# Optimization experiments

Hardware: AMD Instinct MI355X
Metric: run time of the kernel (lower is better)

## Reference

```python
import jax, jax.numpy as jnp
import numpy as np

N = 20000      # nodes
E = 256000     # edges
H = 8          # heads
DIN = 256      # in_dim_struct / in_dim_semantic
DH = 32        # num_hidden per head (H*DH == DIN for GT residual)
PRED = 32      # pred_dim (relation embedding dim)
REL = 16       # rel_num
NEG = 0.2      # negative_slope for GAT attention
ALPHA = 0.5    # args.fusion
NUM_LAYERS = 2


def seg_softmax(e, seg, n):
    # softmax over edges grouped by destination node; e: [E, ...], seg: [E]
    m = jax.ops.segment_max(e, seg, num_segments=n)
    ex = jnp.exp(e - m[seg])
    s = jax.ops.segment_sum(ex, seg, num_segments=n)
    return ex / (s[seg] + 1e-9)


def setup_inputs() -> dict:
    key = jax.random.key(0)
    ks = jax.random.split(key, 24)
    f32 = jnp.float32
    def rn(k, shape, scale=0.05):
        return jax.random.normal(k, shape, dtype=f32) * scale
    return {
        "feats_struct": jax.random.normal(ks[0], (N, DIN), f32),
        "feats_semantic": jax.random.normal(ks[1], (N, DIN), f32),
        "centrality": jax.random.uniform(ks[2], (N,), f32),
        # fused per-head scoring MLP (heads[0] small Sequentials batched over H)
        "Ws1": rn(ks[3], (H, DIN, DIN // 2)),
        "bs1": jnp.zeros((H, DIN // 2), f32),
        "Ws2": rn(ks[4], (H, DIN // 2)),
        "bs2": jnp.zeros((H,), f32),
        "rel_emb": rn(ks[5], (REL, PRED), 1.0),
        # SALayer params (2 layers, per-head scalar channels)
        "sa_w": rn(ks[6], (NUM_LAYERS, H), 1.0),
        "sa_al": rn(ks[7], (NUM_LAYERS, H), 1.0),
        "sa_ar": rn(ks[8], (NUM_LAYERS, H), 1.0),
        "sa_We": rn(ks[9], (NUM_LAYERS, PRED, H)),
        # GTLayer params
        "Wq": rn(ks[10], (DIN, H * DH)),
        "bq": jnp.zeros((H * DH,), f32),
        "Wk": rn(ks[11], (DIN, H * DH)),
        "bk": jnp.zeros((H * DH,), f32),
        "Wv": rn(ks[12], (DIN, H * DH)),
        "bv": jnp.zeros((H * DH,), f32),
        "We_gt": rn(ks[13], (PRED, H * DH)),
        "bn_gamma": jnp.ones((H * DH,), f32),
        "bn_beta": jnp.zeros((H * DH,), f32),
        "Wout": rn(ks[14], (H * DH, 1)),
        "bout": jnp.zeros((1,), f32),
        # centrality scale params
        "gamma": jnp.ones((1, H), f32),
        "beta": jnp.zeros((1, H), f32),
        "edge_types": jax.random.randint(ks[15], (E,), 0, REL),
        "edge_src": jax.random.randint(ks[16], (E,), 0, N),
        "edge_dst": jax.random.randint(ks[17], (E,), 0, N),
    }


def _forward(feats_struct, feats_semantic, centrality, Ws1, bs1, Ws2, bs2,
             rel_emb, sa_w, sa_al, sa_ar, sa_We, Wq, bq, Wk, bk, Wv, bv,
             We_gt, bn_gamma, bn_beta, Wout, bout, gamma, beta,
             edge_types, edge_src, edge_dst):
    n = feats_struct.shape[0]
    edge_feats = rel_emb[edge_types]                                   # [E, PRED]

    # ---- structural channel: fused per-head scoring MLPs ----
    h1 = jax.nn.relu(jnp.einsum('nd,hdk->nhk', feats_struct, Ws1) + bs1)  # [N,H,DIN/2]
    h = jnp.einsum('nhk,hk->nh', h1, Ws2) + bs2                           # [N,H]

    # ---- SALayer stack (GAT-style, per-head scalar features) ----
    for l in range(NUM_LAYERS):
        z = h * sa_w[l]                                                 # [N,H]
        e = jax.nn.leaky_relu(z[edge_src] * sa_al[l] + z[edge_dst] * sa_ar[l]
                              + edge_feats @ sa_We[l], NEG)             # [E,H]
        attn = seg_softmax(e, edge_dst, n)                              # [E,H]
        out = jax.ops.segment_sum(attn * z[edge_src], edge_dst, num_segments=n)
        h = jax.nn.elu(out + z)                                         # residual + activation
        if l != NUM_LAYERS - 1:
            h = jnp.mean(h, axis=-1, keepdims=True)
            h = jnp.tile(h, (1, H))
    logits_struct = h                                                   # [N,H]

    # ---- semantic channel: Graph Transformer layer (edge_mode='MUL') ----
    q = (feats_semantic @ Wq + bq).reshape(n, H, DH)
    k = (feats_semantic @ Wk + bk).reshape(n, H, DH)
    v = (feats_semantic @ Wv + bv).reshape(n, H, DH)
    ep = (edge_feats @ We_gt).reshape(-1, H, DH)                        # [E,H,DH]
    ke = k[edge_src] * ep                                               # MUL edge gating
    score = jnp.sum(q[edge_dst] * ke, axis=-1) / jnp.sqrt(jnp.float32(DH))  # [E,H]
    attn = seg_softmax(score, edge_dst, n)                              # [E,H]
    agg = jax.ops.segment_sum(attn[..., None] * v[edge_src], edge_dst,
                              num_segments=n).reshape(n, H * DH)
    agg = agg + feats_semantic                                          # residual (H*DH == DIN)
    mu = jnp.mean(agg, axis=0)
    var = jnp.var(agg, axis=0)
    agg = (agg - mu) / jnp.sqrt(var + 1e-5) * bn_gamma + bn_beta        # batch norm
    h_sem = jax.nn.relu(agg)
    logits_semantic = h_sem @ Wout + bout                               # [N,1]

    # ---- fusion + centrality gamma/beta scaling ----
    logits = ALPHA * logits_struct + (1.0 - ALPHA) * logits_semantic    # [N,H]
    scaled = (centrality[:, None] * gamma + beta) * logits              # [N,H]
    return jax.nn.leaky_relu(jnp.mean(scaled, axis=-1, keepdims=True), 0.01)


def reference(feats_struct, feats_semantic, centrality, Ws1, bs1, Ws2, bs2,
              rel_emb, sa_w, sa_al, sa_ar, sa_We, Wq, bq, Wk, bk, Wv, bv,
              We_gt, bn_gamma, bn_beta, Wout, bout, gamma, beta,
              edge_types, edge_src, edge_dst):
    return _forward(feats_struct, feats_semantic, centrality, Ws1, bs1, Ws2, bs2,
                    rel_emb, sa_w, sa_al, sa_ar, sa_We, Wq, bq, Wk, bk, Wv, bv,
                    We_gt, bn_gamma, bn_beta, Wout, bout, gamma, beta,
                    edge_types, edge_src, edge_dst)
```

## Files before the change

### kernel.cpp

```cpp
#include <hip/hip_runtime.h>
#include <hip/hip_bf16.h>
#include <math.h>

#define N_NODES 20000
#define N_EDGES 256000
#define LOG2E 1.4426950408889634f

typedef __attribute__((ext_vector_type(8))) __bf16 bf16x8;
typedef __attribute__((ext_vector_type(8))) unsigned short u16x8;
typedef __attribute__((ext_vector_type(4))) float f32x4;

static __device__ __forceinline__ unsigned short f2bf(float f) {
  unsigned u = __float_as_uint(f);
  unsigned r = (u + 0x7fffu + ((u >> 16) & 1u)) >> 16;
  return (unsigned short)r;
}
static __device__ __forceinline__ float b2f(unsigned short u) {
  return __uint_as_float((unsigned)u << 16);
}

__global__ __launch_bounds__(256) void k_setup(
    const float* __restrict__ rel_emb, const float* __restrict__ sa_We,
    const float* __restrict__ We_gt, const float* __restrict__ Xs,
    const float* __restrict__ Xm, const float* __restrict__ Ws1,
    const float* __restrict__ Wq, const float* __restrict__ Wk,
    const float* __restrict__ Wv, const int* __restrict__ e_dst,
    float* __restrict__ saTab, float* __restrict__ epTab,
    ushort* __restrict__ Xsb, ushort* __restrict__ Xmb,
    ushort* __restrict__ Ws1t, ushort* __restrict__ Wt,
    int* __restrict__ deg) {
  int b = blockIdx.x;
  int t = threadIdx.x;
  if (b == 0) {
    {
      int l = t >> 7, r = (t >> 3) & 15, h = t & 7;
      float acc = 0.f;
      for (int p = 0; p < 32; ++p)
        acc += rel_emb[r * 32 + p] * sa_We[l * 256 + p * 8 + h];
      saTab[t] = acc * LOG2E;
    }
    for (int r = 0; r < 16; ++r) {
      float acc = 0.f;
      for (int p = 0; p < 32; ++p)
        acc += rel_emb[r * 32 + p] * We_gt[p * 256 + t];
      epTab[r * 256 + t] = acc;
    }
  } else if (b < 5001) {
    size_t i = ((size_t)(b - 1) * 256 + t) * 4;
    float4 a = *(const float4*)(Xs + i);
    ushort4 ua = {f2bf(a.x), f2bf(a.y), f2bf(a.z), f2bf(a.w)};
    *(ushort4*)(Xsb + i) = ua;
    float4 c = *(const float4*)(Xm + i);
    ushort4 uc = {f2bf(c.x), f2bf(c.y), f2bf(c.z), f2bf(c.w)};
    *(ushort4*)(Xmb + i) = uc;
  } else if (b < 6025) {
    int lb = b - 5001;
    int h = lb >> 7, kcol = lb & 127;
    Ws1t[((size_t)h * 128 + kcol) * 256 + t] =
        f2bf(Ws1[((size_t)h * 256 + t) * 128 + kcol]);
  } else if (b < 6793) {
    int lb = b - 6025;
    int m = lb >> 8, n = lb & 255;
    const float* W = (m == 0) ? Wq : (m == 1) ? Wk : Wv;
    Wt[((size_t)m * 256 + n) * 256 + t] = f2bf(W[(size_t)t * 256 + n]);
  } else {
    int e = (b - 6793) * 256 + t;
    if (e < N_EDGES) atomicAdd(&deg[e_dst[e]], 1);
  }
}

__global__ __launch_bounds__(1024) void k_scan(const int* __restrict__ deg,
                                               int* __restrict__ rowPtr,
                                               int* __restrict__ cursor) {
  const int CH = (N_NODES + 1023) / 1024;
  int t = threadIdx.x;
  int b0 = t * CH, b1 = min(b0 + CH, N_NODES);
  int s = 0;
  for (int i = b0; i < b1; ++i) s += deg[i];
  __shared__ int part[1024];
  part[t] = s;
  __syncthreads();
  for (int off = 1; off < 1024; off <<= 1) {
    int add = (t >= off) ? part[t - off] : 0;
    __syncthreads();
    part[t] += add;
    __syncthreads();
  }
  int run = (t == 0) ? 0 : part[t - 1];
  for (int i = b0; i < b1; ++i) {
    rowPtr[i] = run;
    cursor[i] = run;
    run += deg[i];
  }
  if (t == 0) rowPtr[N_NODES] = part[1023];
}

__global__ void k_fill(const int* __restrict__ e_dst, const int* __restrict__ e_src,
                       const int* __restrict__ e_type, int* __restrict__ cursor,
                       int2* __restrict__ csrPack) {
  int e = blockIdx.x * 256 + threadIdx.x;
  if (e >= N_EDGES) return;
  int d = e_dst[e];
  int pos = atomicAdd(&cursor[d], 1);
  csrPack[pos] = make_int2(e_src[e], e_type[e]);
}

__global__ __launch_bounds__(256) void k_gemm(
    const ushort* __restrict__ Xsb, const ushort* __restrict__ Xmb,
    const ushort* __restrict__ Ws1t, const ushort* __restrict__ Wqkvt,
    const float* __restrict__ bs1, const float* __restrict__ Ws2,
    const float* __restrict__ bs2, const float* __restrict__ bq,
    const float* __restrict__ bk, const float* __restrict__ bv,
    float* __restrict__ h0, float* __restrict__ q, ushort* __restrict__ kvB) {
  __shared__ ushort Ab[64][136];
  __shared__ ushort Bb[128][136];
  int tid = threadIdx.x;
  int y = blockIdx.y;
  bool isMlp = (y < 8);
  int m = 0, half = 0;
  const ushort* Bsrc;
  const ushort* Xb;
  if (isMlp) {
    Xb = Xsb;
    Bsrc = Ws1t + (size_t)y * 128 * 256;
  } else {
    m = (y - 8) >> 1;
    half = (y - 8) & 1;
    Xb = Xmb;
    Bsrc = Wqkvt + ((size_t)m * 256 + half * 128) * 256;
  }
  int base = blockIdx.x * 64;
  int wv = tid >> 6, lane = tid & 63;
  int l15 = lane & 15, lhi = lane >> 4;
  f32x4 acc[8];
  #pragma unroll
  for (int nt = 0; nt < 8; ++nt) acc[nt] = (f32x4){0.f, 0.f, 0.f, 0.f};

  for (int kc = 0; kc < 2; ++kc) {
    {
      int r = tid >> 2, c4 = (tid & 3) * 4;
      int gr = base + r;
      const ushort* src = Xb + (size_t)gr * 256 + kc * 128;
      #pragma unroll
      for (int s = 0; s < 4; ++s) {
        u16x8 val = {0, 0, 0, 0, 0, 0, 0, 0};
        if (gr < N_NODES) val = *(const u16x8*)(src + (c4 + s) * 8);
        *(u16x8*)&Ab[r][(c4 + s) * 8] = val;
      }
    }
    {
      int r = tid >> 1, cb = (tid & 1) * 8;
      const ushort* src = Bsrc + (size_t)r * 256 + kc * 128;
      #pragma unroll
      for (int s = 0; s < 8; ++s)
        *(u16x8*)&Bb[r][(cb + s) * 8] = *(const u16x8*)(src + (cb + s) * 8);
    }
    __syncthreads();
    #pragma unroll
    for (int kk = 0; kk < 4; ++kk) {
      bf16x8 a = *(const bf16x8*)&Ab[wv * 16 + l15][kk * 32 + lhi * 8];
      #pragma unroll
      for (int nt = 0; nt < 8; ++nt) {
        bf16x8 b = *(const bf16x8*)&Bb[nt * 16 + l15][kk * 32 + lhi * 8];
        acc[nt] = __builtin_amdgcn_mfma_f32_16x16x32_bf16(a, b, acc[nt], 0, 0, 0);
      }
    }
    __syncthreads();
  }

  if (isMlp) {
    float part[4] = {0.f, 0.f, 0.f, 0.f};
    #pragma unroll
    for (int nt = 0; nt < 8; ++nt) {
      int c = y * 128 + nt * 16 + l15;
      float b1 = bs1[c], w2 = Ws2[c];
      #pragma unroll
      for (int j = 0; j < 4; ++j)
        part[j] += fmaxf(acc[nt][j] + b1, 0.f) * w2;
    }
    #pragma unroll
    for (int j = 0; j < 4; ++j) {
      #pragma unroll
      for (int o = 1; o < 16; o <<= 1) part[j] += __shfl_xor(part[j], o);
    }
    if (l15 == 0) {
      float b2 = bs2[y];
      #pragma unroll
      for (int j = 0; j < 4; ++j) {
        int row = base + wv * 16 + lhi * 4 + j;
        if (row < N_NODES) h0[(size_t)row * 8 + y] = part[j] + b2;
      }
    }
  } else {
    const float* bias = (m == 0) ? bq : (m == 1) ? bk : bv;
    #pragma unroll
    for (int nt = 0; nt < 8; ++nt) {
      int c = half * 128 + nt * 16 + l15;
      float bc = bias[c];
      #pragma unroll
      for (int j = 0; j < 4; ++j) {
        int row = base + wv * 16 + lhi * 4 + j;
        if (row < N_NODES) {
          float val = acc[nt][j] + bc;
          if (m == 0) q[(size_t)row * 256 + c] = val;
          else if (m == 1) kvB[(size_t)row * 512 + c] = f2bf(val);
          else kvB[(size_t)row * 512 + 256 + c] = f2bf(val);
        }
      }
    }
  }
}


__global__ __launch_bounds__(256) void k_sa(const float* __restrict__ h_in,
                                            float* __restrict__ h_out,
                                            const int* __restrict__ rowPtr,
                                            const int2* __restrict__ csrPack,
                                            const float* __restrict__ sa_w,
                                            const float* __restrict__ sa_al,
                                            const float* __restrict__ sa_ar,
                                            const float* __restrict__ saTab, int layer) {
  int node = blockIdx.x * 4 + (threadIdx.x >> 6);
  int lane = threadIdx.x & 63;
  int h = lane & 7, eslot = lane >> 3;
  float wgt = sa_w[layer * 8 + h];
  float al2 = sa_al[layer * 8 + h] * LOG2E;
  float ar2 = sa_ar[layer * 8 + h] * LOG2E;
  const float* tab = saTab + layer * 128;
  float zd = h_in[(size_t)node * 8 + h] * wgt;
  int s0 = rowPtr[node], s1 = rowPtr[node + 1];
  float m = -1e30f, lsum = 0.f, acc = 0.f;
  for (int i = s0 + eslot; i < s1; i += 8) {
    int2 p = csrPack[i];
    float zs = h_in[(size_t)p.x * 8 + h] * wgt;
    float e = zs * al2 + zd * ar2 + tab[p.y * 8 + h];
    e = (e >= 0.f) ? e : 0.2f * e;
    float nm = fmaxf(m, e);
    float scl = exp2f(m - nm);
    float pw = exp2f(e - nm);
    acc = acc * scl + pw * zs;
    lsum = lsum * scl + pw;
    m = nm;
  }
  #pragma unroll
  for (int off = 8; off < 64; off <<= 1) {
    float om = __shfl_xor(m, off);
    float ol = __shfl_xor(lsum, off);
    float oa = __shfl_xor(acc, off);
    float nm = fmaxf(m, om);
    float sl = exp2f(m - nm);
    float so = exp2f(om - nm);
    acc = acc * sl + oa * so;
    lsum = lsum * sl + ol * so;
    m = nm;
  }
  float o = acc / (lsum + 1e-9f);
  float r = o + zd;
  r = (r > 0.f) ? r : expm1f(r);
  if (layer == 0) {
    r += __shfl_xor(r, 1);
    r += __shfl_xor(r, 2);
    r += __shfl_xor(r, 4);
    r *= 0.125f;
  }
  if (eslot == 0) h_out[(size_t)node * 8 + h] = r;
}


__global__ __launch_bounds__(256) void k_gt(const float* __restrict__ q,
                                            const ushort* __restrict__ kvB,
                                            const float* __restrict__ epTab,
                                            const float* __restrict__ feats_sem,
                                            const int* __restrict__ rowPtr,
                                            const int2* __restrict__ csrPack,
                                            ushort* __restrict__ agg) {
  int node = blockIdx.x * 4 + (threadIdx.x >> 6);
  int lane = threadIdx.x & 63;
  int c0 = lane * 4;
  const float SC2 = 0.17677669529663687f * LOG2E;
  float4 qv = *(const float4*)(q + (size_t)node * 256 + c0);
  qv.x *= SC2; qv.y *= SC2; qv.z *= SC2; qv.w *= SC2;
  float4 acc = {0.f, 0.f, 0.f, 0.f};
  float m = -1e30f, lsum = 0.f;
  int s0 = rowPtr[node], s1 = rowPtr[node + 1];
  int i = s0;
  for (; i + 1 < s1; i += 2) {
    int2 eA = csrPack[i], eB = csrPack[i + 1];
    const ushort* rA = kvB + (size_t)eA.x * 512 + c0;
    const ushort* rB = kvB + (size_t)eB.x * 512 + c0;
    ushort4 kA = *(const ushort4*)rA;
    ushort4 kB4 = *(const ushort4*)rB;
    float4 epA = *(const float4*)(epTab + eA.y * 256 + c0);
    float4 epB = *(const float4*)(epTab + eB.y * 256 + c0);
    ushort4 vA = *(const ushort4*)(rA + 256);
    ushort4 vB = *(const ushort4*)(rB + 256);
    float pA = qv.x * b2f(kA.x) * epA.x + qv.y * b2f(kA.y) * epA.y +
               qv.z * b2f(kA.z) * epA.z + qv.w * b2f(kA.w) * epA.w;
    float pB = qv.x * b2f(kB4.x) * epB.x + qv.y * b2f(kB4.y) * epB.y +
               qv.z * b2f(kB4.z) * epB.z + qv.w * b2f(kB4.w) * epB.w;
    pA += __shfl_xor(pA, 1); pB += __shfl_xor(pB, 1);
    pA += __shfl_xor(pA, 2); pB += __shfl_xor(pB, 2);
    pA += __shfl_xor(pA, 4); pB += __shfl_xor(pB, 4);
    float nm = fmaxf(m, fmaxf(pA, pB));
    float scl = exp2f(m - nm);
    float wA = exp2f(pA - nm);
    float wB = exp2f(pB - nm);
    acc.x = acc.x * scl + wA * b2f(vA.x) + wB * b2f(vB.x);
    acc.y = acc.y * scl + wA * b2f(vA.y) + wB * b2f(vB.y);
    acc.z = acc.z * scl + wA * b2f(vA.z) + wB * b2f(vB.z);
    acc.w = acc.w * scl + wA * b2f(vA.w) + wB * b2f(vB.w);
    lsum = lsum * scl + wA + wB;
    m = nm;
  }
  if (i < s1) {
    int2 eA = csrPack[i];
    const ushort* rA = kvB + (size_t)eA.x * 512 + c0;
    ushort4 kv = *(const ushort4*)rA;
    float4 ep = *(const float4*)(epTab + eA.y * 256 + c0);
    ushort4 vv = *(const ushort4*)(rA + 256);
    float part = qv.x * b2f(kv.x) * ep.x + qv.y * b2f(kv.y) * ep.y +
                 qv.z * b2f(kv.z) * ep.z + qv.w * b2f(kv.w) * ep.w;
    part += __shfl_xor(part, 1);
    part += __shfl_xor(part, 2);
    part += __shfl_xor(part, 4);
    float nm = fmaxf(m, part);
    float scl = exp2f(m - nm);
    float pw = exp2f(part - nm);
    acc.x = acc.x * scl + pw * b2f(vv.x);
    acc.y = acc.y * scl + pw * b2f(vv.y);
    acc.z = acc.z * scl + pw * b2f(vv.z);
    acc.w = acc.w * scl + pw * b2f(vv.w);
    lsum = lsum * scl + pw;
    m = nm;
  }
  float inv = 1.f / (lsum + 1e-9f);
  float4 fs = *(const float4*)(feats_sem + (size_t)node * 256 + c0);
  ushort4 r;
  r.x = f2bf(acc.x * inv + fs.x);
  r.y = f2bf(acc.y * inv + fs.y);
  r.z = f2bf(acc.z * inv + fs.z);
  r.w = f2bf(acc.w * inv + fs.w);
  *(ushort4*)(agg + (size_t)node * 256 + c0) = r;
}

__global__ void k_bnstats(const ushort* __restrict__ agg, double* __restrict__ colsum,
                          double* __restrict__ colssq) {
  int t = threadIdx.x;
  int r0 = blockIdx.x * 79;
  int r1 = min(r0 + 79, N_NODES);
  double s = 0.0, qq = 0.0;
  for (int r = r0; r < r1; ++r) {
    float x = b2f(agg[(size_t)r * 256 + t]);
    s += (double)x;
    qq += (double)x * (double)x;
  }
  atomicAdd(&colsum[t], s);
  atomicAdd(&colssq[t], qq);
}

__global__ void k_bnfinal(const double* __restrict__ colsum, const double* __restrict__ colssq,
                          float* __restrict__ muArr, float* __restrict__ invArr) {
  int t = threadIdx.x;
  double mu = colsum[t] / (double)N_NODES;
  double var = colssq[t] / (double)N_NODES - mu * mu;
  muArr[t] = (float)mu;
  invArr[t] = (float)(1.0 / sqrt(var + 1e-5));
}

__global__ __launch_bounds__(256) void k_final(const ushort* __restrict__ agg,
                                               const float* __restrict__ muArr,
                                               const float* __restrict__ invArr,
                                               const float* __restrict__ bn_gamma,
                                               const float* __restrict__ bn_beta,
                                               const float* __restrict__ Wout,
                                               const float* __restrict__ bout,
                                               const float* __restrict__ hB,
                                               const float* __restrict__ cent,
                                               const float* __restrict__ gamma,
                                               const float* __restrict__ beta,
                                               float* __restrict__ out) {
  int node = blockIdx.x * 4 + (threadIdx.x >> 6);
  int lane = threadIdx.x & 63;
  int c0 = lane * 4;
  ushort4 xa = *(const ushort4*)(agg + (size_t)node * 256 + c0);
  float4 mu = *(const float4*)(muArr + c0);
  float4 iv = *(const float4*)(invArr + c0);
  float4 g = *(const float4*)(bn_gamma + c0);
  float4 b = *(const float4*)(bn_beta + c0);
  float4 w = *(const float4*)(Wout + c0);
  float p = fmaxf((b2f(xa.x) - mu.x) * iv.x * g.x + b.x, 0.f) * w.x +
            fmaxf((b2f(xa.y) - mu.y) * iv.y * g.y + b.y, 0.f) * w.y +
            fmaxf((b2f(xa.z) - mu.z) * iv.z * g.z + b.z, 0.f) * w.z +
            fmaxf((b2f(xa.w) - mu.w) * iv.w * g.w + b.w, 0.f) * w.w;
  #pragma unroll
  for (int o = 1; o < 64; o <<= 1) p += __shfl_xor(p, o);
  float ls = p + bout[0];
  int h = lane & 7;
  float logit = 0.5f * hB[(size_t)node * 8 + h] + 0.5f * ls;
  float sc = (cent[node] * gamma[h] + beta[h]) * logit;
  sc += __shfl_xor(sc, 1);
  sc += __shfl_xor(sc, 2);
  sc += __shfl_xor(sc, 4);
  float mn = sc * 0.125f;
  mn = (mn >= 0.f) ? mn : 0.01f * mn;
  if (lane == 0) out[node] = mn;
}


extern "C" void kernel_launch(void* const* d_in, const int* in_sizes, int n_in,
                              void* d_out, int out_size, void* d_ws, size_t ws_size,
                              hipStream_t stream) {
  (void)in_sizes; (void)n_in; (void)out_size; (void)ws_size;
  const float* feats_struct = (const float*)d_in[0];
  const float* feats_sem    = (const float*)d_in[1];
  const float* cent         = (const float*)d_in[2];
  const float* Ws1          = (const float*)d_in[3];
  const float* bs1          = (const float*)d_in[4];
  const float* Ws2          = (const float*)d_in[5];
  const float* bs2          = (const float*)d_in[6];
  const float* rel_emb      = (const float*)d_in[7];
  const float* sa_w         = (const float*)d_in[8];
  const float* sa_al        = (const float*)d_in[9];
  const float* sa_ar        = (const float*)d_in[10];
  const float* sa_We        = (const float*)d_in[11];
  const float* Wq           = (const float*)d_in[12];
  const float* bq           = (const float*)d_in[13];
  const float* Wk           = (const float*)d_in[14];
  const float* bk           = (const float*)d_in[15];
  const float* Wv           = (const float*)d_in[16];
  const float* bv           = (const float*)d_in[17];
  const float* We_gt        = (const float*)d_in[18];
  const float* bn_gamma     = (const float*)d_in[19];
  const float* bn_beta      = (const float*)d_in[20];
  const float* Wout         = (const float*)d_in[21];
  const float* bout         = (const float*)d_in[22];
  const float* gamma        = (const float*)d_in[23];
  const float* beta         = (const float*)d_in[24];
  const int* e_type         = (const int*)d_in[25];
  const int* e_src          = (const int*)d_in[26];
  const int* e_dst          = (const int*)d_in[27];
  float* out = (float*)d_out;

  char* wsb = (char*)d_ws;
  size_t off = 0;
  auto alloc = [&](size_t bytes) -> char* {
    char* p = wsb + off;
    off = (off + bytes + 255) & ~(size_t)255;
    return p;
  };
  float* saTab   = (float*)alloc(2 * 16 * 8 * 4);
  float* epTab   = (float*)alloc(16 * 256 * 4);
  int* deg       = (int*)alloc((size_t)N_NODES * 4);
  int* rowPtr    = (int*)alloc((size_t)(N_NODES + 1) * 4);
  int* cursor    = (int*)alloc((size_t)N_NODES * 4);
  int2* csrPack  = (int2*)alloc((size_t)N_EDGES * 8);
  float* h0      = (float*)alloc((size_t)N_NODES * 8 * 4);
  float* hA      = (float*)alloc((size_t)N_NODES * 8 * 4);
  float* hB      = (float*)alloc((size_t)N_NODES * 8 * 4);
  float* qb      = (float*)alloc((size_t)N_NODES * 256 * 4);
  ushort* kvB    = (ushort*)alloc((size_t)N_NODES * 512 * 2);
  ushort* agg    = (ushort*)alloc((size_t)N_NODES * 256 * 2);
  double* colsum = (double*)alloc(256 * 8);
  double* colssq = (double*)alloc(256 * 8);
  float* muArr   = (float*)alloc(256 * 4);
  float* invArr  = (float*)alloc(256 * 4);
  ushort* Xsb    = (ushort*)alloc((size_t)N_NODES * 256 * 2);
  ushort* Xmb    = (ushort*)alloc((size_t)N_NODES * 256 * 2);
  ushort* Ws1t   = (ushort*)alloc((size_t)8 * 128 * 256 * 2);
  ushort* Wqkvt  = (ushort*)alloc((size_t)3 * 256 * 256 * 2);

  hipMemsetAsync(deg, 0, (size_t)N_NODES * 4, stream);
  hipMemsetAsync(colsum, 0, 256 * 8, stream);
  hipMemsetAsync(colssq, 0, 256 * 8, stream);

  k_setup<<<7793, 256, 0, stream>>>(rel_emb, sa_We, We_gt, feats_struct, feats_sem,
                                    Ws1, Wq, Wk, Wv, e_dst,
                                    saTab, epTab, Xsb, Xmb, Ws1t, Wqkvt, deg);
  k_scan<<<1, 1024, 0, stream>>>(deg, rowPtr, cursor);
  k_fill<<<(N_EDGES + 255) / 256, 256, 0, stream>>>(e_dst, e_src, e_type, cursor, csrPack);

  const int MT = (N_NODES + 63) / 64;
  dim3 gGemm(MT, 14);
  k_gemm<<<gGemm, 256, 0, stream>>>(Xsb, Xmb, Ws1t, Wqkvt, bs1, Ws2, bs2,
                                    bq, bk, bv, h0, qb, kvB);
  k_sa<<<(N_NODES + 3) / 4, 256, 0, stream>>>(h0, hA, rowPtr, csrPack,
                                              sa_w, sa_al, sa_ar, saTab, 0);
  k_sa<<<(N_NODES + 3) / 4, 256, 0, stream>>>(hA, hB, rowPtr, csrPack,
                                              sa_w, sa_al, sa_ar, saTab, 1);
  k_gt<<<N_NODES / 4, 256, 0, stream>>>(qb, kvB, epTab, feats_sem,
                                        rowPtr, csrPack, agg);
  k_bnstats<<<256, 256, 0, stream>>>(agg, colsum, colssq);
  k_bnfinal<<<1, 256, 0, stream>>>(colsum, colssq, muArr, invArr);
  k_final<<<N_NODES / 4, 256, 0, stream>>>(agg, muArr, invArr, bn_gamma, bn_beta,
                                           Wout, bout, hB, cent, gamma, beta, out);
}
```

Baseline: 367.1 us.

## Enlarge GEMM M-tile to 128 rows and swizzle LDS to avoid bank conflicts

The fused MLP/QKV GEMM kernel now processes 128 rows per block instead of 64, with each wave computing two 16-row MFMA tiles that share each B fragment, so B reuse doubles and weight tile reloads are halved. LDS padding is replaced by an XOR swizzle on the column index to cut bank conflicts while keeping a dense 128-wide layout. The cost is more accumulator registers per thread and half as many blocks in the grid, which lowers parallelism for a 20000-row problem.

```diff
diff --git a/kernel.cpp b/kernel.cpp
--- a/kernel.cpp
+++ b/kernel.cpp
@@ -112,8 +112,8 @@
     const float* __restrict__ bs2, const float* __restrict__ bq,
     const float* __restrict__ bk, const float* __restrict__ bv,
     float* __restrict__ h0, float* __restrict__ q, ushort* __restrict__ kvB) {
-  __shared__ ushort Ab[64][136];
-  __shared__ ushort Bb[128][136];
+  __shared__ ushort Ab[128][128];
+  __shared__ ushort Bb[128][128];
   int tid = threadIdx.x;
   int y = blockIdx.y;
   bool isMlp = (y < 8);
@@ -129,67 +129,78 @@
     Xb = Xmb;
     Bsrc = Wqkvt + ((size_t)m * 256 + half * 128) * 256;
   }
-  int base = blockIdx.x * 64;
+  int base = blockIdx.x * 128;
   int wv = tid >> 6, lane = tid & 63;
   int l15 = lane & 15, lhi = lane >> 4;
-  f32x4 acc[8];
+  int rs = tid >> 4;
+  int cs = (tid & 15) * 8;
+  f32x4 acc[2][8];
   #pragma unroll
-  for (int nt = 0; nt < 8; ++nt) acc[nt] = (f32x4){0.f, 0.f, 0.f, 0.f};
+  for (int mr = 0; mr < 2; ++mr)
+    #pragma unroll
+    for (int nt = 0; nt < 8; ++nt) acc[mr][nt] = (f32x4){0.f, 0.f, 0.f, 0.f};
 
   for (int kc = 0; kc < 2; ++kc) {
-    {
-      int r = tid >> 2, c4 = (tid & 3) * 4;
+    #pragma unroll
+    for (int s = 0; s < 8; ++s) {
+      int r = rs + s * 16;
+      int csw = cs ^ ((r & 7) << 3);
       int gr = base + r;
-      const ushort* src = Xb + (size_t)gr * 256 + kc * 128;
-      #pragma unroll
-      for (int s = 0; s < 4; ++s) {
-        u16x8 val = {0, 0, 0, 0, 0, 0, 0, 0};
-        if (gr < N_NODES) val = *(const u16x8*)(src + (c4 + s) * 8);
-        *(u16x8*)&Ab[r][(c4 + s) * 8] = val;
-      }
-    }
-    {
-      int r = tid >> 1, cb = (tid & 1) * 8;
-      const ushort* src = Bsrc + (size_t)r * 256 + kc * 128;
-      #pragma unroll
-      for (int s = 0; s < 8; ++s)
-        *(u16x8*)&Bb[r][(cb + s) * 8] = *(const u16x8*)(src + (cb + s) * 8);
+      u16x8 val = {0, 0, 0, 0, 0, 0, 0, 0};
+      if (gr < N_NODES) val = *(const u16x8*)(Xb + (size_t)gr * 256 + kc * 128 + cs);
+      *(u16x8*)&Ab[r][csw] = val;
+    }
+    #pragma unroll
+    for (int s = 0; s < 8; ++s) {
+      int r = rs + s * 16;
+      int csw = cs ^ ((r & 7) << 3);
+      *(u16x8*)&Bb[r][csw] = *(const u16x8*)(Bsrc + (size_t)r * 256 + kc * 128 + cs);
     }
     __syncthreads();
+    int swzA = (l15 & 7) << 3;
     #pragma unroll
     for (int kk = 0; kk < 4; ++kk) {
-      bf16x8 a = *(const bf16x8*)&Ab[wv * 16 + l15][kk * 32 + lhi * 8];
+      int col = (kk * 32 + lhi * 8);
+      bf16x8 a0 = *(const bf16x8*)&Ab[wv * 32 + l15][col ^ swzA];
+      bf16x8 a1 = *(const bf16x8*)&Ab[wv * 32 + 16 + l15][col ^ swzA];
       #pragma unroll
       for (int nt = 0; nt < 8; ++nt) {
-        bf16x8 b = *(const bf16x8*)&Bb[nt * 16 + l15][kk * 32 + lhi * 8];
-        acc[nt] = __builtin_amdgcn_mfma_f32_16x16x32_bf16(a, b, acc[nt], 0, 0, 0);
+        bf16x8 b = *(const bf16x8*)&Bb[nt * 16 + l15][col ^ swzA];
+        acc[0][nt] = __builtin_amdgcn_mfma_f32_16x16x32_bf16(a0, b, acc[0][nt], 0, 0, 0);
+        acc[1][nt] = __builtin_amdgcn_mfma_f32_16x16x32_bf16(a1, b, acc[1][nt], 0, 0, 0);
       }
     }
     __syncthreads();
   }
 
   if (isMlp) {
-    float part[4] = {0.f, 0.f, 0.f, 0.f};
+    float part[2][4] = {{0.f, 0.f, 0.f, 0.f}, {0.f, 0.f, 0.f, 0.f}};
     #pragma unroll
     for (int nt = 0; nt < 8; ++nt) {
       int c = y * 128 + nt * 16 + l15;
       float b1 = bs1[c], w2 = Ws2[c];
       #pragma unroll
-      for (int j = 0; j < 4; ++j)
-        part[j] += fmaxf(acc[nt][j] + b1, 0.f) * w2;
-    }
-    #pragma unroll
-    for (int j = 0; j < 4; ++j) {
+      for (int mr = 0; mr < 2; ++mr)
+        #pragma unroll
+        for (int j = 0; j < 4; ++j)
+          part[mr][j] += fmaxf(acc[mr][nt][j] + b1, 0.f) * w2;
+    }
+    #pragma unroll
+    for (int mr = 0; mr < 2; ++mr)
       #pragma unroll
-      for (int o = 1; o < 16; o <<= 1) part[j] += __shfl_xor(part[j], o);
-    }
+      for (int j = 0; j < 4; ++j) {
+        #pragma unroll
+        for (int o = 1; o < 16; o <<= 1) part[mr][j] += __shfl_xor(part[mr][j], o);
+      }
     if (l15 == 0) {
       float b2 = bs2[y];
       #pragma unroll
-      for (int j = 0; j < 4; ++j) {
-        int row = base + wv * 16 + lhi * 4 + j;
-        if (row < N_NODES) h0[(size_t)row * 8 + y] = part[j] + b2;
-      }
+      for (int mr = 0; mr < 2; ++mr)
+        #pragma unroll
+        for (int j = 0; j < 4; ++j) {
+          int row = base + wv * 32 + mr * 16 + lhi * 4 + j;
+          if (row < N_NODES) h0[(size_t)row * 8 + y] = part[mr][j] + b2;
+        }
     }
   } else {
     const float* bias = (m == 0) ? bq : (m == 1) ? bk : bv;
@@ -198,15 +209,17 @@
       int c = half * 128 + nt * 16 + l15;
       float bc = bias[c];
       #pragma unroll
-      for (int j = 0; j < 4; ++j) {
-        int row = base + wv * 16 + lhi * 4 + j;
-        if (row < N_NODES) {
-          float val = acc[nt][j] + bc;
-          if (m == 0) q[(size_t)row * 256 + c] = val;
-          else if (m == 1) kvB[(size_t)row * 512 + c] = f2bf(val);
-          else kvB[(size_t)row * 512 + 256 + c] = f2bf(val);
+      for (int mr = 0; mr < 2; ++mr)
+        #pragma unroll
+        for (int j = 0; j < 4; ++j) {
+          int row = base + wv * 32 + mr * 16 + lhi * 4 + j;
+          if (row < N_NODES) {
+            float val = acc[mr][nt][j] + bc;
+            if (m == 0) q[(size_t)row * 256 + c] = val;
+            else if (m == 1) kvB[(size_t)row * 512 + c] = f2bf(val);
+            else kvB[(size_t)row * 512 + 256 + c] = f2bf(val);
+          }
         }
-      }
     }
   }
 }
@@ -479,7 +492,7 @@
   k_scan<<<1, 1024, 0, stream>>>(deg, rowPtr, cursor);
   k_fill<<<(N_EDGES + 255) / 256, 256, 0, stream>>>(e_dst, e_src, e_type, cursor, csrPack);
 
-  const int MT = (N_NODES + 63) / 64;
+  const int MT = (N_NODES + 127) / 128;
   dim3 gGemm(MT, 14);
   k_gemm<<<gGemm, 256, 0, stream>>>(Xsb, Xmb, Ws1t, Wqkvt, bs1, Ws2, bs2,
                                     bq, bk, bv, h0, qb, kvB);
```

Result: no change. 363.9 us (-0.9%).

## Tile weight transposes through LDS and enlarge GEMM tile with swizzled full-K staging

Applied to the files above, without the earlier changes.

The weight transpose-and-convert in the setup kernel now uses 32x32 LDS tiles, so both reads and writes are coalesced and far fewer blocks are needed. The GEMM kernel moves to 512 threads and 128-row tiles. It loads the whole K=256 slice of A and B into LDS at once, using an XOR swizzle instead of padding to avoid bank conflicts, and drops the two-stage K loop and its extra barriers. The cost is about 128KB of LDS per block, which limits occupancy to one block per CU. The epilogue must still map correctly onto the larger tile and the extra waves.

```diff
diff --git a/kernel.cpp b/kernel.cpp
--- a/kernel.cpp
+++ b/kernel.cpp
@@ -29,6 +29,7 @@
     ushort* __restrict__ Xsb, ushort* __restrict__ Xmb,
     ushort* __restrict__ Ws1t, ushort* __restrict__ Wt,
     int* __restrict__ deg) {
+  __shared__ float tl[32][33];
   int b = blockIdx.x;
   int t = threadIdx.x;
   if (b == 0) {
@@ -45,26 +46,45 @@
         acc += rel_emb[r * 32 + p] * We_gt[p * 256 + t];
       epTab[r * 256 + t] = acc;
     }
-  } else if (b < 5001) {
-    size_t i = ((size_t)(b - 1) * 256 + t) * 4;
+  } else if (b < 449) {
+    int lb = b - 1;
+    int r = t >> 5, c = t & 31;
+    if (lb < 256) {
+      int h = lb >> 5, idx = lb & 31;
+      int k0 = (idx >> 3) * 32, d0 = (idx & 7) * 32;
+      const float* src = Ws1 + (size_t)h * 32768;
+      #pragma unroll
+      for (int i = 0; i < 4; ++i)
+        tl[r + i * 8][c] = src[(size_t)(d0 + r + i * 8) * 128 + k0 + c];
+      __syncthreads();
+      ushort* dst = Ws1t + (size_t)h * 32768;
+      #pragma unroll
+      for (int i = 0; i < 4; ++i)
+        dst[(size_t)(k0 + r + i * 8) * 256 + d0 + c] = f2bf(tl[c][r + i * 8]);
+    } else {
+      int qi = lb - 256;
+      int m = qi >> 6, idx = qi & 63;
+      int n0 = (idx >> 3) * 32, d0 = (idx & 7) * 32;
+      const float* src = (m == 0) ? Wq : (m == 1) ? Wk : Wv;
+      #pragma unroll
+      for (int i = 0; i < 4; ++i)
+        tl[r + i * 8][c] = src[(size_t)(d0 + r + i * 8) * 256 + n0 + c];
+      __syncthreads();
+      ushort* dst = Wt + (size_t)m * 65536;
+      #pragma unroll
+      for (int i = 0; i < 4; ++i)
+        dst[(size_t)(n0 + r + i * 8) * 256 + d0 + c] = f2bf(tl[c][r + i * 8]);
+    }
+  } else if (b < 5449) {
+    size_t i = ((size_t)(b - 449) * 256 + t) * 4;
     float4 a = *(const float4*)(Xs + i);
     ushort4 ua = {f2bf(a.x), f2bf(a.y), f2bf(a.z), f2bf(a.w)};
     *(ushort4*)(Xsb + i) = ua;
-    float4 c = *(const float4*)(Xm + i);
-    ushort4 uc = {f2bf(c.x), f2bf(c.y), f2bf(c.z), f2bf(c.w)};
+    float4 c4 = *(const float4*)(Xm + i);
+    ushort4 uc = {f2bf(c4.x), f2bf(c4.y), f2bf(c4.z), f2bf(c4.w)};
     *(ushort4*)(Xmb + i) = uc;
-  } else if (b < 6025) {
-    int lb = b - 5001;
-    int h = lb >> 7, kcol = lb & 127;
-    Ws1t[((size_t)h * 128 + kcol) * 256 + t] =
-        f2bf(Ws1[((size_t)h * 256 + t) * 128 + kcol]);
-  } else if (b < 6793) {
-    int lb = b - 6025;
-    int m = lb >> 8, n = lb & 255;
-    const float* W = (m == 0) ? Wq : (m == 1) ? Wk : Wv;
-    Wt[((size_t)m * 256 + n) * 256 + t] = f2bf(W[(size_t)t * 256 + n]);
   } else {
-    int e = (b - 6793) * 256 + t;
+    int e = (b - 5449) * 256 + t;
     if (e < N_EDGES) atomicAdd(&deg[e_dst[e]], 1);
   }
 }
@@ -105,15 +125,15 @@
   csrPack[pos] = make_int2(e_src[e], e_type[e]);
 }
 
-__global__ __launch_bounds__(256) void k_gemm(
+__global__ __launch_bounds__(512) void k_gemm(
     const ushort* __restrict__ Xsb, const ushort* __restrict__ Xmb,
     const ushort* __restrict__ Ws1t, const ushort* __restrict__ Wqkvt,
     const float* __restrict__ bs1, const float* __restrict__ Ws2,
     const float* __restrict__ bs2, const float* __restrict__ bq,
     const float* __restrict__ bk, const float* __restrict__ bv,
     float* __restrict__ h0, float* __restrict__ q, ushort* __restrict__ kvB) {
-  __shared__ ushort Ab[64][136];
-  __shared__ ushort Bb[128][136];
+  __shared__ ushort Ab[128][256];
+  __shared__ ushort Bb[128][256];
   int tid = threadIdx.x;
   int y = blockIdx.y;
   bool isMlp = (y < 8);
@@ -124,48 +144,48 @@
     Xb = Xsb;
     Bsrc = Ws1t + (size_t)y * 128 * 256;
   } else {
-    m = (y - 8) >> 1;
-    half = (y - 8) & 1;
+    int s = y - 8;
+    m = s >> 1;
+    half = s & 1;
     Xb = Xmb;
     Bsrc = Wqkvt + ((size_t)m * 256 + half * 128) * 256;
   }
-  int base = blockIdx.x * 64;
+  int base = blockIdx.x * 128;
+
+  {
+    int r = tid >> 2, cq = (tid & 3) * 8;
+    int gr = base + r;
+    const ushort* asrc = Xb + (size_t)gr * 256;
+    const ushort* bsrc = Bsrc + (size_t)r * 256;
+    int sw = (r & 7) << 3;
+    #pragma unroll
+    for (int s = 0; s < 8; ++s) {
+      int colc = (cq + s) * 8;
+      int csw = colc ^ sw;
+      u16x8 av = {0, 0, 0, 0, 0, 0, 0, 0};
+      if (gr < N_NODES) av = *(const u16x8*)(asrc + colc);
+      *(u16x8*)&Ab[r][csw] = av;
+      *(u16x8*)&Bb[r][csw] = *(const u16x8*)(bsrc + colc);
+    }
+  }
+  __syncthreads();
+
   int wv = tid >> 6, lane = tid & 63;
   int l15 = lane & 15, lhi = lane >> 4;
+  int swzA = (l15 & 7) << 3;
   f32x4 acc[8];
   #pragma unroll
   for (int nt = 0; nt < 8; ++nt) acc[nt] = (f32x4){0.f, 0.f, 0.f, 0.f};
 
-  for (int kc = 0; kc < 2; ++kc) {
-    {
-      int r = tid >> 2, c4 = (tid & 3) * 4;
-      int gr = base + r;
-      const ushort* src = Xb + (size_t)gr * 256 + kc * 128;
-      #pragma unroll
-      for (int s = 0; s < 4; ++s) {
-        u16x8 val = {0, 0, 0, 0, 0, 0, 0, 0};
-        if (gr < N_NODES) val = *(const u16x8*)(src + (c4 + s) * 8);
-        *(u16x8*)&Ab[r][(c4 + s) * 8] = val;
-      }
-    }
-    {
-      int r = tid >> 1, cb = (tid & 1) * 8;
-      const ushort* src = Bsrc + (size_t)r * 256 + kc * 128;
-      #pragma unroll
-      for (int s = 0; s < 8; ++s)
-        *(u16x8*)&Bb[r][(cb + s) * 8] = *(const u16x8*)(src + (cb + s) * 8);
-    }
-    __syncthreads();
+  #pragma unroll
+  for (int kk = 0; kk < 8; ++kk) {
+    int col = kk * 32 + lhi * 8;
+    bf16x8 a = *(const bf16x8*)&Ab[wv * 16 + l15][col ^ swzA];
     #pragma unroll
-    for (int kk = 0; kk < 4; ++kk) {
-      bf16x8 a = *(const bf16x8*)&Ab[wv * 16 + l15][kk * 32 + lhi * 8];
-      #pragma unroll
-      for (int nt = 0; nt < 8; ++nt) {
-        bf16x8 b = *(const bf16x8*)&Bb[nt * 16 + l15][kk * 32 + lhi * 8];
-        acc[nt] = __builtin_amdgcn_mfma_f32_16x16x32_bf16(a, b, acc[nt], 0, 0, 0);
-      }
-    }
-    __syncthreads();
+    for (int nt = 0; nt < 8; ++nt) {
+      bf16x8 b = *(const bf16x8*)&Bb[nt * 16 + l15][col ^ swzA];
+      acc[nt] = __builtin_amdgcn_mfma_f32_16x16x32_bf16(a, b, acc[nt], 0, 0, 0);
+    }
   }
 
   if (isMlp) {
@@ -473,15 +493,15 @@
   hipMemsetAsync(colsum, 0, 256 * 8, stream);
   hipMemsetAsync(colssq, 0, 256 * 8, stream);
 
-  k_setup<<<7793, 256, 0, stream>>>(rel_emb, sa_We, We_gt, feats_struct, feats_sem,
+  k_setup<<<6449, 256, 0, stream>>>(rel_emb, sa_We, We_gt, feats_struct, feats_sem,
                                     Ws1, Wq, Wk, Wv, e_dst,
                                     saTab, epTab, Xsb, Xmb, Ws1t, Wqkvt, deg);
   k_scan<<<1, 1024, 0, stream>>>(deg, rowPtr, cursor);
   k_fill<<<(N_EDGES + 255) / 256, 256, 0, stream>>>(e_dst, e_src, e_type, cursor, csrPack);
 
-  const int MT = (N_NODES + 63) / 64;
+  const int MT = (N_NODES + 127) / 128;
   dim3 gGemm(MT, 14);
-  k_gemm<<<gGemm, 256, 0, stream>>>(Xsb, Xmb, Ws1t, Wqkvt, bs1, Ws2, bs2,
+  k_gemm<<<gGemm, 512, 0, stream>>>(Xsb, Xmb, Ws1t, Wqkvt, bs1, Ws2, bs2,
                                     bq, bk, bv, h0, qb, kvB);
   k_sa<<<(N_NODES + 3) / 4, 256, 0, stream>>>(h0, hA, rowPtr, csrPack,
                                               sa_w, sa_al, sa_ar, saTab, 0);
```

Result: slower. 414.2 us (+12.8%).
